# Kernel tuning notes

Measured on AMD Instinct MI355X. Metric: run time of the kernel, lower is better.

## Reference

```python
import jax, jax.numpy as jnp
import numpy as np

B, WIN, NN, NF, NH, NOUT = 4, 10, 10000, 8, 64, 1
N = B * WIN * NN          # stacked graph nodes
E = 3200000               # edges
EPS = 1e-5                # BatchNorm eps


def _gcn(x, edge_index, ew, W, b):
    # PyG GCNConv: linear first, then sym-normalized aggregation with self loops.
    xl = x @ W  # [N, H]
    loop = jnp.arange(N)
    row = jnp.concatenate([edge_index[0], loop])
    col = jnp.concatenate([edge_index[1], loop])
    w = jnp.concatenate([ew, jnp.ones((N,), ew.dtype)])
    deg = jax.ops.segment_sum(w, col, num_segments=N)
    dinv = jnp.where(deg > 0, jax.lax.rsqrt(deg), 0.0)
    norm = dinv[row] * w * dinv[col]
    out = jax.ops.segment_sum(norm[:, None] * xl[row], col, num_segments=N)
    return out + b


def _bn(x, g, bta):
    # training-mode BatchNorm1d (batch statistics, biased variance)
    m = x.mean(0)
    v = x.var(0)
    return (x - m) * jax.lax.rsqrt(v + EPS) * g + bta


def _lstm(xs, wih, whh, bih, bhh):
    # xs: [T, Bn, D]; PyTorch gate order i, f, g, o
    H = whh.shape[1]
    Bn = xs.shape[1]
    h0 = jnp.zeros((Bn, H), xs.dtype)
    c0 = jnp.zeros((Bn, H), xs.dtype)
    def step(carry, xt):
        h, c = carry
        gates = xt @ wih.T + bih + h @ whh.T + bhh
        i, f, g, o = jnp.split(gates, 4, axis=-1)
        c = jax.nn.sigmoid(f) * c + jax.nn.sigmoid(i) * jnp.tanh(g)
        h = jax.nn.sigmoid(o) * jnp.tanh(c)
        return (h, c), h
    (hn, cn), ys = jax.lax.scan(step, (h0, c0), xs)
    return ys, hn


def setup_inputs() -> dict:
    key = jax.random.key(0)
    ks = jax.random.split(key, 16)
    def rn(k, shape, s=0.05):
        return jax.random.normal(k, shape, jnp.float32) * s
    return {
        "x": jax.random.normal(ks[0], (N, NF), jnp.float32),
        "edge_index": jax.random.randint(ks[1], (2, E), 0, N),
        "edge_weight": jax.random.uniform(ks[2], (E,), jnp.float32),
        "c1_w": rn(ks[3], (NF, NH)), "c1_b": jnp.zeros((NH,), jnp.float32),
        "c2_w": rn(ks[4], (NH, NH)), "c2_b": jnp.zeros((NH,), jnp.float32),
        "bn1_g": jnp.ones((NH,), jnp.float32), "bn1_b": jnp.zeros((NH,), jnp.float32),
        "bn2_g": jnp.ones((NH,), jnp.float32), "bn2_b": jnp.zeros((NH,), jnp.float32),
        "l1_wih": rn(ks[5], (4 * NH, 2 * NH)), "l1_whh": rn(ks[6], (4 * NH, NH)),
        "l1_bih": jnp.zeros((4 * NH,), jnp.float32), "l1_bhh": jnp.zeros((4 * NH,), jnp.float32),
        "l2_wih": rn(ks[7], (4 * NH, NH)), "l2_whh": rn(ks[8], (4 * NH, NH)),
        "l2_bih": jnp.zeros((4 * NH,), jnp.float32), "l2_bhh": jnp.zeros((4 * NH,), jnp.float32),
        "fc1_w": rn(ks[9], (NH, 2 * NH + WIN * NF)), "fc1_b": jnp.zeros((NH,), jnp.float32),
        "fc2_w": rn(ks[10], (NOUT, NH)), "fc2_b": jnp.zeros((NOUT,), jnp.float32),
    }


def reference(x, edge_index, edge_weight, c1_w, c1_b, c2_w, c2_b,
              bn1_g, bn1_b, bn2_g, bn2_b,
              l1_wih, l1_whh, l1_bih, l1_bhh,
              l2_wih, l2_whh, l2_bih, l2_bhh,
              fc1_w, fc1_b, fc2_w, fc2_b):
    # skip connection: raw features per (batch,node) over the window
    skip = x.reshape(B, WIN, NN, NF).transpose(0, 2, 1, 3).reshape(B * NN, WIN * NF)
    # two GCN layers (dropout is identity in deterministic/eval reference)
    h1 = _bn(jax.nn.relu(_gcn(x, edge_index, edge_weight, c1_w, c1_b)), bn1_g, bn1_b)
    h2 = _bn(jax.nn.relu(_gcn(h1, edge_index, edge_weight, c2_w, c2_b)), bn2_g, bn2_b)
    xc = jnp.concatenate([h1, h2], axis=1)  # [N, 2H]
    xr = xc.reshape(B, WIN, NN, 2 * NH).transpose(1, 0, 2, 3).reshape(WIN, B * NN, 2 * NH)
    ys1, hn1 = _lstm(xr, l1_wih, l1_whh, l1_bih, l1_bhh)
    ys2, hn2 = _lstm(ys1, l2_wih, l2_whh, l2_bih, l2_bhh)
    z = jnp.concatenate([hn1, hn2, skip], axis=1)
    z = jax.nn.relu(z @ fc1_w.T + fc1_b)
    z = jax.nn.relu(z @ fc2_w.T + fc2_b)
    return z.reshape(-1)
```

## Files before the change

kernel.cpp:

```cpp
#include <hip/hip_runtime.h>
#include <math.h>

constexpr int BB     = 4;
constexpr int WINN   = 10;
constexpr int NNODES = 10000;
constexpr int NFEAT  = 8;
constexpr int NHID   = 64;
constexpr int NTOT   = BB * WINN * NNODES;
constexpr int NEDGE  = 3200000;
constexpr int NBN    = BB * NNODES;
constexpr float EPSBN = 1e-5f;

#define DEVFN static __device__ __forceinline__

typedef float f4 __attribute__((ext_vector_type(4)));
typedef short s8v __attribute__((ext_vector_type(8)));
typedef unsigned short ushort_t;
typedef unsigned int uint_t;

DEVFN float sigmoidf_(float x) { return 1.0f / (1.0f + __expf(-x)); }
DEVFN float tanhf_(float x) { return 2.0f / (1.0f + __expf(-2.0f * x)) - 1.0f; }
DEVFN ushort_t f2bf(float f) {
    uint_t x = __float_as_uint(f);
    return (ushort_t)((x + 0x7FFFu + ((x >> 16) & 1u)) >> 16);
}
DEVFN float bf2f(ushort_t u) { return __uint_as_float(((uint_t)u) << 16); }

__global__ void k_diag(float* out, float wsz, int n) {
    int i = blockIdx.x * 256 + threadIdx.x;
    if (i < n) out[i] = wsz;
}

__global__ void k_init(int* cntP, float* sums) {
    int i = blockIdx.x * 256 + threadIdx.x;
    if (i < 8 * NTOT) cntP[i] = 0;
    if (i < 2048) sums[i] = 0.f;
}

__global__ void k_hist(const int* __restrict__ ei, int* __restrict__ cntP) {
    int e = blockIdx.x * 256 + threadIdx.x;
    int p = blockIdx.x & 7;
    if (e < NEDGE) atomicAdd(&cntP[p * NTOT + ei[NEDGE + e]], 1);
}

__global__ void k_scan1(const int* __restrict__ cntP, int* __restrict__ ptr, int* __restrict__ tmp) {
    __shared__ int sdat[256];
    int tid = threadIdx.x;
    int base = blockIdx.x * 1024 + tid * 4;
    int v[4];
#pragma unroll
    for (int j = 0; j < 4; ++j) {
        int idx = base + j;
        int s = 0;
        if (idx < NTOT) {
#pragma unroll
            for (int p = 0; p < 8; ++p) s += cntP[p * NTOT + idx];
        }
        v[j] = s;
    }
    int sum = v[0] + v[1] + v[2] + v[3];
    sdat[tid] = sum;
    __syncthreads();
    for (int ofs = 1; ofs < 256; ofs <<= 1) {
        int x = (tid >= ofs) ? sdat[tid - ofs] : 0;
        __syncthreads();
        sdat[tid] += x;
        __syncthreads();
    }
    int run = sdat[tid] - sum;
    if (base + 0 < NTOT) ptr[base + 0] = run; run += v[0];
    if (base + 1 < NTOT) ptr[base + 1] = run; run += v[1];
    if (base + 2 < NTOT) ptr[base + 2] = run; run += v[2];
    if (base + 3 < NTOT) ptr[base + 3] = run;
    if (tid == 255) tmp[blockIdx.x] = sdat[255];
}

__global__ void k_scan2(int* tmp, int nb) {
    __shared__ int st[512];
    int tid = threadIdx.x;
    int v = (tid < nb) ? tmp[tid] : 0;
    st[tid] = v;
    __syncthreads();
    for (int ofs = 1; ofs < 512; ofs <<= 1) {
        int x = (tid >= ofs) ? st[tid - ofs] : 0;
        __syncthreads();
        st[tid] += x;
        __syncthreads();
    }
    if (tid < nb) tmp[tid] = st[tid] - v;
}

__global__ void k_scan3(int* __restrict__ ptr, int* __restrict__ cntP, const int* __restrict__ tmp) {
    int i = blockIdx.x * 256 + threadIdx.x;
    if (i < NTOT) {
        int p0 = ptr[i] + tmp[i >> 10];
        ptr[i] = p0;
        int run = p0;
#pragma unroll
        for (int p = 0; p < 8; ++p) {
            int c = cntP[p * NTOT + i];
            cntP[p * NTOT + i] = run;
            run += c;
        }
    }
    if (i == 0) ptr[NTOT] = NEDGE;
}

__global__ void k_fill(const int* __restrict__ ei, const float* __restrict__ ew,
                       int* __restrict__ cur8, int2* __restrict__ epack) {
    int e = blockIdx.x * 256 + threadIdx.x;
    if (e >= NEDGE) return;
    int p = blockIdx.x & 7;
    int row = ei[e], col = ei[NEDGE + e];
    int pos = atomicAdd(&cur8[p * NTOT + col], 1);
    epack[pos] = make_int2(row, __float_as_int(ew[e]));
}

__global__ void k_degcsr(const int* __restrict__ ptr, const int2* __restrict__ epack,
                         float* __restrict__ dinv) {
    int tid = threadIdx.x;
    int lane = tid & 63;
    int waveg = blockIdx.x * 4 + (tid >> 6);
    int g = lane >> 3, sub = lane & 7;
    int node = waveg * 8 + g;
    int beg = ptr[node], end = ptr[node + 1];
    float s = 0.f;
    for (int e = beg + sub; e < end; e += 8) s += __int_as_float(epack[e].y);
    s += __shfl_xor(s, 1, 64);
    s += __shfl_xor(s, 2, 64);
    s += __shfl_xor(s, 4, 64);
    if (sub == 0) dinv[node] = rsqrtf(1.0f + s);
}

__global__ void k_gather8(const int* __restrict__ ptr, const int2* __restrict__ epack,
                          const float* __restrict__ x, const float* __restrict__ dinv,
                          float* __restrict__ aggX) {
    int tid = threadIdx.x;
    int lane = tid & 63;
    int waveg = blockIdx.x * 4 + (tid >> 6);
    int g = lane >> 3, ch = lane & 7;
    int node = waveg * 8 + g;
    int beg = ptr[node], end = ptr[node + 1];
    float dv = dinv[node];
    float accE = 0.f;
    int e = beg;
    for (; e + 3 < end; e += 4) {
        int2 p0 = epack[e], p1 = epack[e + 1], p2 = epack[e + 2], p3 = epack[e + 3];
        float n0 = dinv[p0.x] * __int_as_float(p0.y);
        float n1 = dinv[p1.x] * __int_as_float(p1.y);
        float n2 = dinv[p2.x] * __int_as_float(p2.y);
        float n3 = dinv[p3.x] * __int_as_float(p3.y);
        accE = fmaf(n0, x[p0.x * 8 + ch], accE);
        accE = fmaf(n1, x[p1.x * 8 + ch], accE);
        accE = fmaf(n2, x[p2.x * 8 + ch], accE);
        accE = fmaf(n3, x[p3.x * 8 + ch], accE);
    }
    for (; e < end; ++e) {
        int2 p = epack[e];
        accE = fmaf(dinv[p.x] * __int_as_float(p.y), x[p.x * 8 + ch], accE);
    }
    aggX[node * 8 + ch] = dv * fmaf(dv, x[node * 8 + ch], accE);
}

__global__ void k_lin1(const float* __restrict__ aggX, const float* __restrict__ W,
                       const float* __restrict__ bias, ushort_t* __restrict__ rbf,
                       float* __restrict__ sums) {
    __shared__ float sW[NFEAT * NHID];
    int tid = threadIdx.x;
    sW[tid] = W[tid];
    sW[tid + 256] = W[tid + 256];
    __syncthreads();
    int c = tid & 63;
    float b = bias[c];
    float s = 0.f, sq = 0.f;
    int stride = gridDim.x * 256;
    for (int i = blockIdx.x * 256 + tid; i < NTOT * 64; i += stride) {
        int n = i >> 6;
        float acc = b;
#pragma unroll
        for (int f = 0; f < NFEAT; ++f) acc = fmaf(aggX[n * NFEAT + f], sW[f * NHID + c], acc);
        acc = acc > 0.f ? acc : 0.f;
        rbf[i] = f2bf(acc);
        s += acc;
        sq = fmaf(acc, acc, sq);
    }
    __shared__ float ls[4][64], lq[4][64];
    int w = tid >> 6;
    ls[w][c] = s; lq[w][c] = sq;
    __syncthreads();
    if (tid < 64) {
        atomicAdd(&sums[tid], ls[0][tid] + ls[1][tid] + ls[2][tid] + ls[3][tid]);
        atomicAdd(&sums[64 + tid], lq[0][tid] + lq[1][tid] + lq[2][tid] + lq[3][tid]);
    }
}

__global__ void k_bn_final(const float* __restrict__ sums, const float* __restrict__ g,
                           const float* __restrict__ b, float* __restrict__ ss) {
    int i = threadIdx.x;
    if (i >= 64) return;
    float mean = sums[i] * (1.0f / NTOT);
    float var = sums[64 + i] * (1.0f / NTOT) - mean * mean;
    float sc = g[i] * rsqrtf(var + EPSBN);
    ss[i] = sc;
    ss[64 + i] = b[i] - mean * sc;
}

__global__ void k_bn_final8(const float* __restrict__ sums8, const float* __restrict__ g,
                            const float* __restrict__ b, float* __restrict__ ss) {
    int i = threadIdx.x;
    if (i >= 64) return;
    float S = 0.f, Q = 0.f;
#pragma unroll
    for (int m = 0; m < 8; ++m) { S += sums8[m * 128 + i]; Q += sums8[m * 128 + 64 + i]; }
    float mean = S * (1.0f / NTOT);
    float var = Q * (1.0f / NTOT) - mean * mean;
    float sc = g[i] * rsqrtf(var + EPSBN);
    ss[i] = sc;
    ss[64 + i] = b[i] - mean * sc;
}

__global__ void k_gather64b(const int* __restrict__ ptr, const int2* __restrict__ epack,
                            const ushort_t* __restrict__ rbf, const float* __restrict__ dinv,
                            const float* __restrict__ ss1, ushort_t* __restrict__ gout) {
    int lane = threadIdx.x & 63;
    int node = blockIdx.x * 4 + (threadIdx.x >> 6);
    int beg = ptr[node], end = ptr[node + 1];
    float dv = dinv[node];
    float accE = 0.f, accS = 0.f;
    int e = beg;
    for (; e + 3 < end; e += 4) {
        int2 p0 = epack[e], p1 = epack[e + 1], p2 = epack[e + 2], p3 = epack[e + 3];
        float n0 = dinv[p0.x] * __int_as_float(p0.y);
        float n1 = dinv[p1.x] * __int_as_float(p1.y);
        float n2 = dinv[p2.x] * __int_as_float(p2.y);
        float n3 = dinv[p3.x] * __int_as_float(p3.y);
        accE = fmaf(n0, bf2f(rbf[(size_t)p0.x * 64 + lane]), accE);
        accE = fmaf(n1, bf2f(rbf[(size_t)p1.x * 64 + lane]), accE);
        accE = fmaf(n2, bf2f(rbf[(size_t)p2.x * 64 + lane]), accE);
        accE = fmaf(n3, bf2f(rbf[(size_t)p3.x * 64 + lane]), accE);
        accS += n0 + n1 + n2 + n3;
    }
    for (; e < end; ++e) {
        int2 p = epack[e];
        float nv = dinv[p.x] * __int_as_float(p.y);
        accE = fmaf(nv, bf2f(rbf[(size_t)p.x * 64 + lane]), accE);
        accS += nv;
    }
    float G = dv * fmaf(dv, bf2f(rbf[(size_t)node * 64 + lane]), accE);
    float S = dv * (dv + accS);
    gout[(size_t)node * 64 + lane] = f2bf(fmaf(ss1[lane], G, ss1[64 + lane] * S));
}

__global__ void k_lin2c(const ushort_t* __restrict__ gin, const float* __restrict__ W2,
                        const float* __restrict__ bias, ushort_t* __restrict__ dst,
                        float* __restrict__ sums8) {
    __shared__ __align__(16) float srow[4][64];
    __shared__ float ls[4][64], lq[4][64];
    int lane = threadIdx.x & 63, wv = threadIdx.x >> 6;
    float wc[64];
#pragma unroll
    for (int h = 0; h < 64; ++h) wc[h] = W2[h * 64 + lane];
    float b = bias[lane];
    float s = 0.f, sq = 0.f;
    int wid = blockIdx.x * 4 + wv;
    int nw = gridDim.x * 4;
    for (int row = wid; row < NTOT; row += nw) {
        srow[wv][lane] = bf2f(gin[(size_t)row * 64 + lane]);
        float acc = b;
#pragma unroll
        for (int h4 = 0; h4 < 16; ++h4) {
            float4 iv = *reinterpret_cast<const float4*>(&srow[wv][h4 * 4]);
            acc = fmaf(iv.x, wc[h4 * 4 + 0], acc);
            acc = fmaf(iv.y, wc[h4 * 4 + 1], acc);
            acc = fmaf(iv.z, wc[h4 * 4 + 2], acc);
            acc = fmaf(iv.w, wc[h4 * 4 + 3], acc);
        }
        acc = acc > 0.f ? acc : 0.f;
        dst[(size_t)row * 64 + lane] = f2bf(acc);
        s += acc;
        sq = fmaf(acc, acc, sq);
    }
    ls[wv][lane] = s; lq[wv][lane] = sq;
    __syncthreads();
    if (threadIdx.x < 64) {
        float S = ls[0][lane] + ls[1][lane] + ls[2][lane] + ls[3][lane];
        float Q = lq[0][lane] + lq[1][lane] + lq[2][lane] + lq[3][lane];
        float* d = sums8 + (blockIdx.x & 7) * 128;
        atomicAdd(&d[lane], S);
        atomicAdd(&d[64 + lane], Q);
    }
}

__global__ void k_prep(const float* __restrict__ wih1, const float* __restrict__ whh1,
                       const float* __restrict__ bih1, const float* __restrict__ bhh1,
                       const float* __restrict__ wih2, const float* __restrict__ whh2,
                       const float* __restrict__ bih2, const float* __restrict__ bhh2,
                       const float* __restrict__ fc1w,
                       float* wB1f, float* b1, ushort_t* wB2h, float* b2, float* fc1T) {
    int i = blockIdx.x * 256 + threadIdx.x;
    if (i < 256 * 192) {
        int n = i / 192, k = i - n * 192;
        wB1f[i] = (k < 128) ? wih1[n * 128 + k] : whh1[n * 64 + (k - 128)];
    }
    if (i < 256 * 128) {
        int n = i >> 7, k = i & 127;
        wB2h[i] = f2bf((k < 64) ? wih2[n * 64 + k] : whh2[n * 64 + (k - 64)]);
    }
    if (i < 208 * 64) {
        int k = i >> 6, o = i & 63;
        fc1T[i] = fc1w[o * 208 + k];
    }
    if (i < 256) { b1[i] = bih1[i] + bhh1[i]; b2[i] = bih2[i] + bhh2[i]; }
}

__global__ void k_fold2(float* __restrict__ wB1f, float* __restrict__ b1,
                        const float* __restrict__ ss1, const float* __restrict__ ss2,
                        ushort_t* __restrict__ wB1h) {
    int n = threadIdx.x;
    float acc = 0.f;
#pragma unroll
    for (int m = 0; m < 64; ++m) {
        float w = wB1f[n * 192 + m];
        acc = fmaf(w, ss1[64 + m], acc);
        wB1f[n * 192 + m] = w * ss1[m];
    }
#pragma unroll
    for (int m = 0; m < 64; ++m) {
        float w = wB1f[n * 192 + 64 + m];
        acc = fmaf(w, ss2[64 + m], acc);
        wB1f[n * 192 + 64 + m] = w * ss2[m];
    }
    b1[n] += acc;
    __syncthreads();
    for (int j = n; j < 256 * 192; j += 256) wB1h[j] = f2bf(wB1f[j]);
}

__global__ __launch_bounds__(256, 1) void k_lstm_mfma4(
    const ushort_t* __restrict__ h1bf, const ushort_t* __restrict__ h2bf,
    const ushort_t* __restrict__ wB1, const ushort_t* __restrict__ wB2,
    const float* __restrict__ bs1, const float* __restrict__ bs2,
    float* __restrict__ hA, float* __restrict__ hB) {
    __shared__ ushort_t hx1[2][1024], hx2[2][1024];
    int tid = threadIdx.x;
    int lane = tid & 63, wv = tid >> 6;
    int c15 = lane & 15, g4 = lane >> 4;
    int g8 = g4 * 8;
    int bn0 = blockIdx.x * 16;
    int b = bn0 / NNODES, nn0 = bn0 - b * NNODES;

    for (int i = tid; i < 2048; i += 256) {
        if (i < 1024) ((uint_t*)hx1)[i] = 0u;
        else ((uint_t*)hx2)[i - 1024] = 0u;
    }

    s8v w1f[4][6], w2f[4][4];
#pragma unroll
    for (int j = 0; j < 4; ++j) {
        const ushort_t* base1 = wB1 + (size_t)((wv + 4 * j) * 16 + c15) * 192 + g8;
#pragma unroll
        for (int kk = 0; kk < 6; ++kk) w1f[j][kk] = *(const s8v*)(base1 + kk * 32);
        const ushort_t* base2 = wB2 + (size_t)((wv + 4 * j) * 16 + c15) * 128 + g8;
#pragma unroll
        for (int kk = 0; kk < 4; ++kk) w2f[j][kk] = *(const s8v*)(base2 + kk * 32);
    }
    float bi1[4], bi2[4];
#pragma unroll
    for (int j = 0; j < 4; ++j) {
        bi1[j] = bs1[(wv + 4 * j) * 16 + c15];
        bi2[j] = bs2[(wv + 4 * j) * 16 + c15];
    }
    float cA[4], cB[4];
#pragma unroll
    for (int q = 0; q < 4; ++q) { cA[q] = 0.f; cB[q] = 0.f; }

    int r7 = c15 & 7;
    int a_lo = c15 * 64 + ((g4 ^ r7) << 3);
    int a_hi = c15 * 64 + (((4 + g4) ^ r7) << 3);
    int u = wv * 16 + c15;
    int hxcol_hi = (u >> 3) << 3;
    int u7 = u & 7;

    size_t nd0 = (size_t)((b * WINN + 0) * NNODES + nn0 + c15) * 64 + g8;
    s8v g0 = *(const s8v*)(h1bf + nd0);
    s8v g1 = *(const s8v*)(h1bf + nd0 + 32);
    s8v g2 = *(const s8v*)(h2bf + nd0);
    s8v g3 = *(const s8v*)(h2bf + nd0 + 32);

    __syncthreads();

    for (int t = 0; t < WINN; ++t) {
        int cur = t & 1, prv = 1 - cur;
        int tn = (t + 1 < WINN) ? t + 1 : t;
        size_t ndn = (size_t)((b * WINN + tn) * NNODES + nn0 + c15) * 64 + g8;
        s8v n0 = *(const s8v*)(h1bf + ndn);
        s8v n1 = *(const s8v*)(h1bf + ndn + 32);
        s8v n2 = *(const s8v*)(h2bf + ndn);
        s8v n3 = *(const s8v*)(h2bf + ndn + 32);

        s8v a4 = *(const s8v*)(&hx1[prv][a_lo]);
        s8v a5 = *(const s8v*)(&hx1[prv][a_hi]);

        f4 acc[4];
#pragma unroll
        for (int j = 0; j < 4; ++j) { f4 v = {bi1[j], bi1[j], bi1[j], bi1[j]}; acc[j] = v; }
#pragma unroll
        for (int j = 0; j < 4; ++j) {
            acc[j] = __builtin_amdgcn_mfma_f32_16x16x32_bf16(g0, w1f[j][0], acc[j], 0, 0, 0);
            acc[j] = __builtin_amdgcn_mfma_f32_16x16x32_bf16(g1, w1f[j][1], acc[j], 0, 0, 0);
            acc[j] = __builtin_amdgcn_mfma_f32_16x16x32_bf16(g2, w1f[j][2], acc[j], 0, 0, 0);
            acc[j] = __builtin_amdgcn_mfma_f32_16x16x32_bf16(g3, w1f[j][3], acc[j], 0, 0, 0);
            acc[j] = __builtin_amdgcn_mfma_f32_16x16x32_bf16(a4, w1f[j][4], acc[j], 0, 0, 0);
            acc[j] = __builtin_amdgcn_mfma_f32_16x16x32_bf16(a5, w1f[j][5], acc[j], 0, 0, 0);
        }
#pragma unroll
        for (int q = 0; q < 4; ++q) {
            float ig = sigmoidf_(acc[0][q]);
            float fg = sigmoidf_(acc[1][q]);
            float gg = tanhf_(acc[2][q]);
            float og = sigmoidf_(acc[3][q]);
            float cv = fmaf(fg, cA[q], ig * gg);
            cA[q] = cv;
            float hv = og * tanhf_(cv);
            int rr = g4 * 4 + q;
            hx1[cur][rr * 64 + (hxcol_hi ^ ((rr & 7) << 3)) + u7] = f2bf(hv);
        }
        __syncthreads();

        s8v r0 = *(const s8v*)(&hx1[cur][a_lo]);
        s8v r1 = *(const s8v*)(&hx1[cur][a_hi]);
        s8v r2 = *(const s8v*)(&hx2[prv][a_lo]);
        s8v r3 = *(const s8v*)(&hx2[prv][a_hi]);
#pragma unroll
        for (int j = 0; j < 4; ++j) { f4 v = {bi2[j], bi2[j], bi2[j], bi2[j]}; acc[j] = v; }
#pragma unroll
        for (int j = 0; j < 4; ++j) {
            acc[j] = __builtin_amdgcn_mfma_f32_16x16x32_bf16(r0, w2f[j][0], acc[j], 0, 0, 0);
            acc[j] = __builtin_amdgcn_mfma_f32_16x16x32_bf16(r1, w2f[j][1], acc[j], 0, 0, 0);
            acc[j] = __builtin_amdgcn_mfma_f32_16x16x32_bf16(r2, w2f[j][2], acc[j], 0, 0, 0);
            acc[j] = __builtin_amdgcn_mfma_f32_16x16x32_bf16(r3, w2f[j][3], acc[j], 0, 0, 0);
        }
#pragma unroll
        for (int q = 0; q < 4; ++q) {
            float ig = sigmoidf_(acc[0][q]);
            float fg = sigmoidf_(acc[1][q]);
            float gg = tanhf_(acc[2][q]);
            float og = sigmoidf_(acc[3][q]);
            float cv = fmaf(fg, cB[q], ig * gg);
            cB[q] = cv;
            float hv = og * tanhf_(cv);
            int rr = g4 * 4 + q;
            hx2[cur][rr * 64 + (hxcol_hi ^ ((rr & 7) << 3)) + u7] = f2bf(hv);
        }
        g0 = n0; g1 = n1; g2 = n2; g3 = n3;
    }
    __syncthreads();
    int fin = (WINN - 1) & 1;
    for (int i = tid; i < 1024; i += 256) {
        int rr = i >> 6, uu = i & 63;
        int hw2 = rr * 64 + ((((uu >> 3) ^ (rr & 7)) << 3)) + (uu & 7);
        hA[(size_t)(bn0 + rr) * 64 + uu] = bf2f(hx1[fin][hw2]);
        hB[(size_t)(bn0 + rr) * 64 + uu] = bf2f(hx2[fin][hw2]);
    }
}

__global__ void k_head(const float* __restrict__ hA, const float* __restrict__ hB,
                       const float* __restrict__ x, const float* __restrict__ fc1T,
                       const float* __restrict__ fc1b, const float* __restrict__ fc2w,
                       const float* __restrict__ fc2b, float* __restrict__ out) {
    int lane = threadIdx.x & 63, wv = threadIdx.x >> 6;
    int bn = blockIdx.x * 4 + wv;
    __shared__ float sz[4][208];
    int b = bn / NNODES, nn = bn - b * NNODES;
    for (int k = lane; k < 208; k += 64) {
        float v;
        if (k < 64) v = hA[(size_t)bn * 64 + k];
        else if (k < 128) v = hB[(size_t)bn * 64 + (k - 64)];
        else {
            int kk = k - 128;
            int w = kk >> 3, f = kk & 7;
            v = x[(size_t)((b * WINN + w) * NNODES + nn) * NFEAT + f];
        }
        sz[wv][k] = v;
    }
    __syncthreads();
    float acc = fc1b[lane];
    for (int k = 0; k < 208; ++k) acc = fmaf(sz[wv][k], fc1T[k * 64 + lane], acc);
    acc = acc > 0.f ? acc : 0.f;
    float v = acc * fc2w[lane];
#pragma unroll
    for (int m = 32; m >= 1; m >>= 1) v += __shfl_xor(v, m, 64);
    if (lane == 0) {
        float z = v + fc2b[0];
        out[bn] = z > 0.f ? z : 0.f;
    }
}

extern "C" void kernel_launch(void* const* d_in, const int* in_sizes, int n_in,
                              void* d_out, int out_size, void* d_ws, size_t ws_size,
                              hipStream_t stream) {
    const float* x     = (const float*)d_in[0];
    const int*   ei    = (const int*)d_in[1];
    const float* ew    = (const float*)d_in[2];
    const float* c1w   = (const float*)d_in[3];
    const float* c1b   = (const float*)d_in[4];
    const float* c2w   = (const float*)d_in[5];
    const float* c2b   = (const float*)d_in[6];
    const float* bn1g  = (const float*)d_in[7];
    const float* bn1b  = (const float*)d_in[8];
    const float* bn2g  = (const float*)d_in[9];
    const float* bn2b  = (const float*)d_in[10];
    const float* wih1  = (const float*)d_in[11];
    const float* whh1  = (const float*)d_in[12];
    const float* bih1  = (const float*)d_in[13];
    const float* bhh1  = (const float*)d_in[14];
    const float* wih2  = (const float*)d_in[15];
    const float* whh2  = (const float*)d_in[16];
    const float* bih2  = (const float*)d_in[17];
    const float* bhh2  = (const float*)d_in[18];
    const float* fc1w  = (const float*)d_in[19];
    const float* fc1b  = (const float*)d_in[20];
    const float* fc2w  = (const float*)d_in[21];
    const float* fc2b  = (const float*)d_in[22];
    float* out = (float*)d_out;

    float* ws = (float*)d_ws;
    size_t off = 0;
    auto A = [&](size_t n) { float* p = ws + off; off += n; return p; };
    float* dinv   = A(NTOT);
    float* aggX   = A((size_t)NTOT * NFEAT);
    ushort_t* h1bf = (ushort_t*)A((size_t)NTOT * 32);
    ushort_t* h2bf = (ushort_t*)A((size_t)NTOT * 32);
    ushort_t* gbuf = (ushort_t*)A((size_t)NTOT * 32);

    size_t uoff = off;
    float* hA = A((size_t)NBN * 64);
    float* hB = A((size_t)NBN * 64);
    A(2 * (size_t)NEDGE + (NTOT + 1) + 8 * (size_t)NTOT - 2 * (size_t)NBN * 64);
    int2* epack = (int2*)(ws + uoff);
    int*  ptr   = (int*)(epack + NEDGE);
    int*  cntP  = ptr + NTOT + 1;

    float* wB1f = A(256 * 192);
    ushort_t* wB1h = (ushort_t*)A(256 * 96);
    ushort_t* wB2h = (ushort_t*)A(256 * 64);
    float* b1   = A(256);
    float* b2   = A(256);
    float* fc1T = A(208 * 64);
    float* sums = A(2048);
    float* ss1  = A(128);
    float* ss2  = A(128);
    float* scanTmpF = A(512);
    int* scanTmp = (int*)scanTmpF;

    if (ws_size < off * sizeof(float)) {
        k_diag<<<(out_size + 255) / 256, 256, 0, stream>>>(out, (float)ws_size, out_size);
        return;
    }

    constexpr int SCAN_NB = (NTOT + 1023) / 1024;

    k_init<<<8 * NTOT / 256, 256, 0, stream>>>(cntP, sums);
    k_hist<<<NEDGE / 256, 256, 0, stream>>>(ei, cntP);
    k_scan1<<<SCAN_NB, 256, 0, stream>>>(cntP, ptr, scanTmp);
    k_scan2<<<1, 512, 0, stream>>>(scanTmp, SCAN_NB);
    k_scan3<<<(NTOT + 255) / 256, 256, 0, stream>>>(ptr, cntP, scanTmp);
    k_fill<<<NEDGE / 256, 256, 0, stream>>>(ei, ew, cntP, epack);
    k_degcsr<<<NTOT / 8 / 4, 256, 0, stream>>>(ptr, epack, dinv);
    k_prep<<<192, 256, 0, stream>>>(wih1, whh1, bih1, bhh1, wih2, whh2, bih2, bhh2,
                                    fc1w, wB1f, b1, wB2h, b2, fc1T);

    k_gather8<<<NTOT / 8 / 4, 256, 0, stream>>>(ptr, epack, x, dinv, aggX);
    k_lin1<<<512, 256, 0, stream>>>(aggX, c1w, c1b, h1bf, sums);
    k_bn_final<<<1, 64, 0, stream>>>(sums, bn1g, bn1b, ss1);

    k_gather64b<<<NTOT / 4, 256, 0, stream>>>(ptr, epack, h1bf, dinv, ss1, gbuf);
    k_lin2c<<<2048, 256, 0, stream>>>(gbuf, c2w, c2b, h2bf, sums + 128);
    k_bn_final8<<<1, 64, 0, stream>>>(sums + 128, bn2g, bn2b, ss2);
    k_fold2<<<1, 256, 0, stream>>>(wB1f, b1, ss1, ss2, wB1h);

    k_lstm_mfma4<<<NBN / 16, 256, 0, stream>>>(h1bf, h2bf, wB1h, wB2h, b1, b2, hA, hB);

    k_head<<<NBN / 4, 256, 0, stream>>>(hA, hB, x, fc1T, fc1b, fc2w, fc2b, out);
}
```

Measured before the change: 1.190 ms.

## Pipeline the two LSTM layers across separate wave groups with a one-step skew

The fused two-layer LSTM kernel now launches 512 threads per block. Four waves compute layer 1 and four compute layer 2, with layer 2 lagging one timestep behind. The layers therefore run concurrently and each step needs one barrier instead of two. Each wave also holds only one layer's weight fragments in registers, which lowers register pressure. In exchange the loop runs one extra step, the block is larger, and the two wave groups do unequal work per step (6 versus 4 MFMAs per gate), so layer-2 waves idle part of the time.

```diff
diff --git a/kernel.cpp b/kernel.cpp
--- a/kernel.cpp
+++ b/kernel.cpp
@@ -335,7 +335,7 @@
     for (int j = n; j < 256 * 192; j += 256) wB1h[j] = f2bf(wB1f[j]);
 }
 
-__global__ __launch_bounds__(256, 1) void k_lstm_mfma4(
+__global__ __launch_bounds__(512, 1) void k_lstm_mfma8(
     const ushort_t* __restrict__ h1bf, const ushort_t* __restrict__ h2bf,
     const ushort_t* __restrict__ wB1, const ushort_t* __restrict__ wB2,
     const float* __restrict__ bs1, const float* __restrict__ bs2,
@@ -347,115 +347,124 @@
     int g8 = g4 * 8;
     int bn0 = blockIdx.x * 16;
     int b = bn0 / NNODES, nn0 = bn0 - b * NNODES;
-
-    for (int i = tid; i < 2048; i += 256) {
-        if (i < 1024) ((uint_t*)hx1)[i] = 0u;
-        else ((uint_t*)hx2)[i - 1024] = 0u;
-    }
-
-    s8v w1f[4][6], w2f[4][4];
-#pragma unroll
-    for (int j = 0; j < 4; ++j) {
-        const ushort_t* base1 = wB1 + (size_t)((wv + 4 * j) * 16 + c15) * 192 + g8;
-#pragma unroll
-        for (int kk = 0; kk < 6; ++kk) w1f[j][kk] = *(const s8v*)(base1 + kk * 32);
-        const ushort_t* base2 = wB2 + (size_t)((wv + 4 * j) * 16 + c15) * 128 + g8;
-#pragma unroll
-        for (int kk = 0; kk < 4; ++kk) w2f[j][kk] = *(const s8v*)(base2 + kk * 32);
-    }
-    float bi1[4], bi2[4];
-#pragma unroll
-    for (int j = 0; j < 4; ++j) {
-        bi1[j] = bs1[(wv + 4 * j) * 16 + c15];
-        bi2[j] = bs2[(wv + 4 * j) * 16 + c15];
-    }
-    float cA[4], cB[4];
-#pragma unroll
-    for (int q = 0; q < 4; ++q) { cA[q] = 0.f; cB[q] = 0.f; }
+    bool isL1 = wv < 4;
+    int n = wv & 3;
+
+    for (int i = tid; i < 1024; i += 512) { ((uint_t*)hx1)[i] = 0u; ((uint_t*)hx2)[i] = 0u; }
+
+    s8v wf[4][6];
+    if (isL1) {
+#pragma unroll
+        for (int g = 0; g < 4; ++g) {
+            const ushort_t* base = wB1 + (size_t)((g * 4 + n) * 16 + c15) * 192 + g8;
+#pragma unroll
+            for (int kk = 0; kk < 6; ++kk) wf[g][kk] = *(const s8v*)(base + kk * 32);
+        }
+    } else {
+#pragma unroll
+        for (int g = 0; g < 4; ++g) {
+            const ushort_t* base = wB2 + (size_t)((g * 4 + n) * 16 + c15) * 128 + g8;
+#pragma unroll
+            for (int kk = 0; kk < 4; ++kk) wf[g][kk] = *(const s8v*)(base + kk * 32);
+        }
+    }
+    float bi[4];
+#pragma unroll
+    for (int g = 0; g < 4; ++g)
+        bi[g] = isL1 ? bs1[(g * 4 + n) * 16 + c15] : bs2[(g * 4 + n) * 16 + c15];
+    float cst[4];
+#pragma unroll
+    for (int q = 0; q < 4; ++q) cst[q] = 0.f;
 
     int r7 = c15 & 7;
     int a_lo = c15 * 64 + ((g4 ^ r7) << 3);
     int a_hi = c15 * 64 + (((4 + g4) ^ r7) << 3);
-    int u = wv * 16 + c15;
+    int u = n * 16 + c15;
     int hxcol_hi = (u >> 3) << 3;
     int u7 = u & 7;
 
-    size_t nd0 = (size_t)((b * WINN + 0) * NNODES + nn0 + c15) * 64 + g8;
-    s8v g0 = *(const s8v*)(h1bf + nd0);
-    s8v g1 = *(const s8v*)(h1bf + nd0 + 32);
-    s8v g2 = *(const s8v*)(h2bf + nd0);
-    s8v g3 = *(const s8v*)(h2bf + nd0 + 32);
-
-    __syncthreads();
-
-    for (int t = 0; t < WINN; ++t) {
-        int cur = t & 1, prv = 1 - cur;
-        int tn = (t + 1 < WINN) ? t + 1 : t;
-        size_t ndn = (size_t)((b * WINN + tn) * NNODES + nn0 + c15) * 64 + g8;
-        s8v n0 = *(const s8v*)(h1bf + ndn);
-        s8v n1 = *(const s8v*)(h1bf + ndn + 32);
-        s8v n2 = *(const s8v*)(h2bf + ndn);
-        s8v n3 = *(const s8v*)(h2bf + ndn + 32);
-
-        s8v a4 = *(const s8v*)(&hx1[prv][a_lo]);
-        s8v a5 = *(const s8v*)(&hx1[prv][a_hi]);
-
-        f4 acc[4];
-#pragma unroll
-        for (int j = 0; j < 4; ++j) { f4 v = {bi1[j], bi1[j], bi1[j], bi1[j]}; acc[j] = v; }
-#pragma unroll
-        for (int j = 0; j < 4; ++j) {
-            acc[j] = __builtin_amdgcn_mfma_f32_16x16x32_bf16(g0, w1f[j][0], acc[j], 0, 0, 0);
-            acc[j] = __builtin_amdgcn_mfma_f32_16x16x32_bf16(g1, w1f[j][1], acc[j], 0, 0, 0);
-            acc[j] = __builtin_amdgcn_mfma_f32_16x16x32_bf16(g2, w1f[j][2], acc[j], 0, 0, 0);
-            acc[j] = __builtin_amdgcn_mfma_f32_16x16x32_bf16(g3, w1f[j][3], acc[j], 0, 0, 0);
-            acc[j] = __builtin_amdgcn_mfma_f32_16x16x32_bf16(a4, w1f[j][4], acc[j], 0, 0, 0);
-            acc[j] = __builtin_amdgcn_mfma_f32_16x16x32_bf16(a5, w1f[j][5], acc[j], 0, 0, 0);
-        }
-#pragma unroll
-        for (int q = 0; q < 4; ++q) {
-            float ig = sigmoidf_(acc[0][q]);
-            float fg = sigmoidf_(acc[1][q]);
-            float gg = tanhf_(acc[2][q]);
-            float og = sigmoidf_(acc[3][q]);
-            float cv = fmaf(fg, cA[q], ig * gg);
-            cA[q] = cv;
-            float hv = og * tanhf_(cv);
-            int rr = g4 * 4 + q;
-            hx1[cur][rr * 64 + (hxcol_hi ^ ((rr & 7) << 3)) + u7] = f2bf(hv);
+    s8v g0, g1, g2, g3;
+    if (isL1) {
+        size_t nd0 = (size_t)((b * WINN + 0) * NNODES + nn0 + c15) * 64 + g8;
+        g0 = *(const s8v*)(h1bf + nd0);
+        g1 = *(const s8v*)(h1bf + nd0 + 32);
+        g2 = *(const s8v*)(h2bf + nd0);
+        g3 = *(const s8v*)(h2bf + nd0 + 32);
+    }
+    __syncthreads();
+
+    for (int s = 0; s <= WINN; ++s) {
+        if (isL1 && s < WINN) {
+            int cur = s & 1, prv = 1 - cur;
+            int tn = (s + 1 < WINN) ? s + 1 : s;
+            size_t ndn = (size_t)((b * WINN + tn) * NNODES + nn0 + c15) * 64 + g8;
+            s8v n0 = *(const s8v*)(h1bf + ndn);
+            s8v n1 = *(const s8v*)(h1bf + ndn + 32);
+            s8v n2 = *(const s8v*)(h2bf + ndn);
+            s8v n3 = *(const s8v*)(h2bf + ndn + 32);
+            s8v a4 = *(const s8v*)(&hx1[prv][a_lo]);
+            s8v a5 = *(const s8v*)(&hx1[prv][a_hi]);
+            f4 acc[4];
+#pragma unroll
+            for (int g = 0; g < 4; ++g) { f4 v = {bi[g], bi[g], bi[g], bi[g]}; acc[g] = v; }
+#pragma unroll
+            for (int g = 0; g < 4; ++g) {
+                acc[g] = __builtin_amdgcn_mfma_f32_16x16x32_bf16(g0, wf[g][0], acc[g], 0, 0, 0);
+                acc[g] = __builtin_amdgcn_mfma_f32_16x16x32_bf16(g1, wf[g][1], acc[g], 0, 0, 0);
+                acc[g] = __builtin_amdgcn_mfma_f32_16x16x32_bf16(g2, wf[g][2], acc[g], 0, 0, 0);
+                acc[g] = __builtin_amdgcn_mfma_f32_16x16x32_bf16(g3, wf[g][3], acc[g], 0, 0, 0);
+                acc[g] = __builtin_amdgcn_mfma_f32_16x16x32_bf16(a4, wf[g][4], acc[g], 0, 0, 0);
+                acc[g] = __builtin_amdgcn_mfma_f32_16x16x32_bf16(a5, wf[g][5], acc[g], 0, 0, 0);
+            }
+#pragma unroll
+            for (int q = 0; q < 4; ++q) {
+                float ig = sigmoidf_(acc[0][q]);
+                float fg = sigmoidf_(acc[1][q]);
+                float gg = tanhf_(acc[2][q]);
+                float og = sigmoidf_(acc[3][q]);
+                float cv = fmaf(fg, cst[q], ig * gg);
+                cst[q] = cv;
+                float hv = og * tanhf_(cv);
+                int rr = g4 * 4 + q;
+                hx1[cur][rr * 64 + (hxcol_hi ^ ((rr & 7) << 3)) + u7] = f2bf(hv);
+            }
+            g0 = n0; g1 = n1; g2 = n2; g3 = n3;
+        }
+        if (!isL1 && s >= 1) {
+            int t2 = s - 1;
+            int c2 = t2 & 1, p2 = 1 - c2;
+            s8v r0 = *(const s8v*)(&hx1[c2][a_lo]);
+            s8v r1 = *(const s8v*)(&hx1[c2][a_hi]);
+            s8v r2 = *(const s8v*)(&hx2[p2][a_lo]);
+            s8v r3 = *(const s8v*)(&hx2[p2][a_hi]);
+            f4 acc[4];
+#pragma unroll
+            for (int g = 0; g < 4; ++g) { f4 v = {bi[g], bi[g], bi[g], bi[g]}; acc[g] = v; }
+#pragma unroll
+            for (int g = 0; g < 4; ++g) {
+                acc[g] = __builtin_amdgcn_mfma_f32_16x16x32_bf16(r0, wf[g][0], acc[g], 0, 0, 0);
+                acc[g] = __builtin_amdgcn_mfma_f32_16x16x32_bf16(r1, wf[g][1], acc[g], 0, 0, 0);
+                acc[g] = __builtin_amdgcn_mfma_f32_16x16x32_bf16(r2, wf[g][2], acc[g], 0, 0, 0);
+                acc[g] = __builtin_amdgcn_mfma_f32_16x16x32_bf16(r3, wf[g][3], acc[g], 0, 0, 0);
+            }
+#pragma unroll
+            for (int q = 0; q < 4; ++q) {
+                float ig = sigmoidf_(acc[0][q]);
+                float fg = sigmoidf_(acc[1][q]);
+                float gg = tanhf_(acc[2][q]);
+                float og = sigmoidf_(acc[3][q]);
+                float cv = fmaf(fg, cst[q], ig * gg);
+                cst[q] = cv;
+                float hv = og * tanhf_(cv);
+                int rr = g4 * 4 + q;
+                hx2[c2][rr * 64 + (hxcol_hi ^ ((rr & 7) << 3)) + u7] = f2bf(hv);
+            }
         }
         __syncthreads();
-
-        s8v r0 = *(const s8v*)(&hx1[cur][a_lo]);
-        s8v r1 = *(const s8v*)(&hx1[cur][a_hi]);
-        s8v r2 = *(const s8v*)(&hx2[prv][a_lo]);
-        s8v r3 = *(const s8v*)(&hx2[prv][a_hi]);
-#pragma unroll
-        for (int j = 0; j < 4; ++j) { f4 v = {bi2[j], bi2[j], bi2[j], bi2[j]}; acc[j] = v; }
-#pragma unroll
-        for (int j = 0; j < 4; ++j) {
-            acc[j] = __builtin_amdgcn_mfma_f32_16x16x32_bf16(r0, w2f[j][0], acc[j], 0, 0, 0);
-            acc[j] = __builtin_amdgcn_mfma_f32_16x16x32_bf16(r1, w2f[j][1], acc[j], 0, 0, 0);
-            acc[j] = __builtin_amdgcn_mfma_f32_16x16x32_bf16(r2, w2f[j][2], acc[j], 0, 0, 0);
-            acc[j] = __builtin_amdgcn_mfma_f32_16x16x32_bf16(r3, w2f[j][3], acc[j], 0, 0, 0);
-        }
-#pragma unroll
-        for (int q = 0; q < 4; ++q) {
-            float ig = sigmoidf_(acc[0][q]);
-            float fg = sigmoidf_(acc[1][q]);
-            float gg = tanhf_(acc[2][q]);
-            float og = sigmoidf_(acc[3][q]);
-            float cv = fmaf(fg, cB[q], ig * gg);
-            cB[q] = cv;
-            float hv = og * tanhf_(cv);
-            int rr = g4 * 4 + q;
-            hx2[cur][rr * 64 + (hxcol_hi ^ ((rr & 7) << 3)) + u7] = f2bf(hv);
-        }
-        g0 = n0; g1 = n1; g2 = n2; g3 = n3;
-    }
-    __syncthreads();
+    }
+
     int fin = (WINN - 1) & 1;
-    for (int i = tid; i < 1024; i += 256) {
+    for (int i = tid; i < 1024; i += 512) {
         int rr = i >> 6, uu = i & 63;
         int hw2 = rr * 64 + ((((uu >> 3) ^ (rr & 7)) << 3)) + (uu & 7);
         hA[(size_t)(bn0 + rr) * 64 + uu] = bf2f(hx1[fin][hw2]);
@@ -578,7 +587,7 @@
     k_bn_final8<<<1, 64, 0, stream>>>(sums + 128, bn2g, bn2b, ss2);
     k_fold2<<<1, 256, 0, stream>>>(wB1f, b1, ss1, ss2, wB1h);
 
-    k_lstm_mfma4<<<NBN / 16, 256, 0, stream>>>(h1bf, h2bf, wB1h, wB2h, b1, b2, hA, hB);
+    k_lstm_mfma8<<<NBN / 16, 512, 0, stream>>>(h1bf, h2bf, wB1h, wB2h, b1, b2, hA, hB);
 
     k_head<<<NBN / 4, 256, 0, stream>>>(hA, hB, x, fc1T, fc1b, fc2w, fc2b, out);
 }
```

Result: faster. 1.150 ms (-3.4%).
